# Kernel optimization log

Hardware: AMD Instinct MI355X
Metric: run time of the kernel (lower is better)

Reference implementation:

```python
import jax, jax.numpy as jnp
import numpy as np

FP8_MAX = 448.0
FP8_HI_PREC_MAX = 224.0
UNC_THRESH = 0.1
EPS = 1e-08


def setup_inputs() -> dict:
    key = jax.random.key(0)
    k1, k2, k3 = jax.random.split(key, 3)
    B, S, H, D, M = 1, 4096, 32, 128, 4096
    return {
        "k": jax.random.normal(k1, (B, S, H, D), dtype=jnp.float32),
        "v": jax.random.normal(k2, (B, S, H, D), dtype=jnp.float32),
        "uncertainty": jax.random.uniform(k3, (B, S), dtype=jnp.float32),
        "k_cache": jnp.zeros((H, M, D), dtype=jnp.float32),
        "v_cache": jnp.zeros((H, M, D), dtype=jnp.float32),
        "k_scales": jnp.ones((H, M), dtype=jnp.float32),
        "v_scales": jnp.ones((H, M), dtype=jnp.float32),
        "current_pos": 0,
    }


def reference(k, v, uncertainty, k_cache, v_cache, k_scales, v_scales, current_pos):
    # k, v: [1, S, H, D]; caches: [H, M, D]; scales: [H, M]
    H, M, D = k_cache.shape
    S = k.shape[1]
    pos = (current_pos + jnp.arange(S)) % M  # circular-buffer write positions

    kt = k[0]  # [S, H, D]
    vt = v[0]

    # per-token fp8 divisor: high-precision range when uncertain
    div = jnp.where(uncertainty[0] > UNC_THRESH, FP8_HI_PREC_MAX, FP8_MAX)  # [S]

    # per-token amax over all heads and dims -> scalar scale per token
    k_s = jnp.maximum(jnp.max(jnp.abs(kt), axis=(1, 2)) / div, EPS)  # [S]
    v_s = jnp.maximum(jnp.max(jnp.abs(vt), axis=(1, 2)) / div, EPS)

    kq = jnp.clip(kt / k_s[:, None, None], -FP8_MAX, FP8_MAX)  # [S, H, D]
    vq = jnp.clip(vt / v_s[:, None, None], -FP8_MAX, FP8_MAX)

    # scatter-append into circular buffer ([H, S, D] layout for cache writes)
    new_k_cache = k_cache.at[:, pos].set(jnp.swapaxes(kq, 0, 1))
    new_v_cache = v_cache.at[:, pos].set(jnp.swapaxes(vq, 0, 1))
    new_k_scales = k_scales.at[:, pos].set(jnp.broadcast_to(k_s, (H, S)))
    new_v_scales = v_scales.at[:, pos].set(jnp.broadcast_to(v_s, (H, S)))
    return (new_k_cache, new_v_cache, new_k_scales, new_v_scales)
```

## Files before the change

kernel.cpp:

```cpp
#include <hip/hip_runtime.h>

#define HH 32
#define DD 128
#define MM 4096
#define ROW_F4 1024
#define D_F4   32

typedef float v4f __attribute__((ext_vector_type(4)));

__global__ __launch_bounds__(256)
void teleport_quant_kernel(const float* __restrict__ kin,
                           const float* __restrict__ vin,
                           const float* __restrict__ unc,
                           const float* __restrict__ kc_in,
                           const float* __restrict__ vc_in,
                           const float* __restrict__ ksc_in,
                           const float* __restrict__ vsc_in,
                           const int*   __restrict__ cur_pos,
                           float* __restrict__ kc_out,
                           float* __restrict__ vc_out,
                           float* __restrict__ ksc_out,
                           float* __restrict__ vsc_out,
                           int S)
{
    const int t    = threadIdx.x;
    const int lane = t & 63;
    const int w    = (blockIdx.x << 2) + (t >> 6);
    const int m    = w >> 1;
    const int isV  = w & 1;

    int cp  = *cur_pos;
    int cpm = cp % MM; if (cpm < 0) cpm += MM;
    int s0  = m - cpm; if (s0 < 0) s0 += MM;
    const int s = (s0 < S) ? (s0 + MM * ((S - 1 - s0) / MM)) : -1;

    const v4f* cin  = reinterpret_cast<const v4f*>(isV ? vc_in : kc_in);
    v4f*       cout = reinterpret_cast<v4f*>(isV ? vc_out : kc_out);
    const float* sin_ = isV ? vsc_in  : ksc_in;
    float*       sout = isV ? vsc_out : ksc_out;

    if (s < 0) {
        #pragma unroll
        for (int c = 0; c < 16; ++c) {
            int f4 = c * 64 + lane;
            int o  = (f4 >> 5) * (MM * D_F4) + m * D_F4 + (f4 & 31);
            cout[o] = cin[o];
        }
        if (lane < HH) sout[lane * MM + m] = sin_[lane * MM + m];
        return;
    }

    const v4f* src = reinterpret_cast<const v4f*>(isV ? vin : kin)
                     + (size_t)s * ROW_F4;

    v4f a[16];
    float am = 0.0f;
    #pragma unroll
    for (int c = 0; c < 16; ++c) {
        a[c] = src[c * 64 + lane];
        am = fmaxf(am, fmaxf(fmaxf(fabsf(a[c].x), fabsf(a[c].y)),
                             fmaxf(fabsf(a[c].z), fabsf(a[c].w))));
    }

    #pragma unroll
    for (int off = 32; off > 0; off >>= 1)
        am = fmaxf(am, __shfl_xor(am, off, 64));

    const float u   = unc[s];
    const float div = (u > 0.1f) ? 224.0f : 448.0f;
    const float sc  = fmaxf(am / div, 1e-8f);
    const float r   = 1.0f / sc;

    #pragma unroll
    for (int c = 0; c < 16; ++c) {
        int f4 = c * 64 + lane;
        int o  = (f4 >> 5) * (MM * D_F4) + m * D_F4 + (f4 & 31);
        v4f q;
        q.x = fminf(fmaxf(a[c].x * r, -448.0f), 448.0f);
        q.y = fminf(fmaxf(a[c].y * r, -448.0f), 448.0f);
        q.z = fminf(fmaxf(a[c].z * r, -448.0f), 448.0f);
        q.w = fminf(fmaxf(a[c].w * r, -448.0f), 448.0f);
        cout[o] = q;
    }

    if (lane < HH) sout[lane * MM + m] = sc;
}

extern "C" void kernel_launch(void* const* d_in, const int* in_sizes, int n_in,
                              void* d_out, int out_size, void* d_ws, size_t ws_size,
                              hipStream_t stream) {
    const float* kin = (const float*)d_in[0];
    const float* vin = (const float*)d_in[1];
    const float* unc = (const float*)d_in[2];
    const float* kc  = (const float*)d_in[3];
    const float* vc  = (const float*)d_in[4];
    const float* ksc = (const float*)d_in[5];
    const float* vsc = (const float*)d_in[6];
    const int*   cp  = (const int*)d_in[7];
    const int S = in_sizes[2];

    float* out  = (float*)d_out;
    float* kco  = out;
    float* vco  = kco + (size_t)HH * MM * DD;
    float* ksco = vco + (size_t)HH * MM * DD;
    float* vsco = ksco + (size_t)HH * MM;

    teleport_quant_kernel<<<(2 * MM) / 4, 256, 0, stream>>>(
        kin, vin, unc, kc, vc, ksc, vsc, cp, kco, vco, ksco, vsco, S);
}
```

Before: 51.86 us.

## Split quantization into scale pass and head-major write pass

Splits the fused kernel into two launches. The first computes per-token scales and reciprocals into workspace; the second reads k/v again and writes the cache in contiguous head-major order. This targets the strided scatter writes of the original per-token layout, at the cost of reading inputs twice and an extra launch.

Result: slower. 69.66 us (+34.3%).

```diff
diff --git a/kernel.cpp b/kernel.cpp
--- a/kernel.cpp
+++ b/kernel.cpp
@@ -9,19 +9,13 @@
 typedef float v4f __attribute__((ext_vector_type(4)));
 
 __global__ __launch_bounds__(256)
-void teleport_quant_kernel(const float* __restrict__ kin,
-                           const float* __restrict__ vin,
-                           const float* __restrict__ unc,
-                           const float* __restrict__ kc_in,
-                           const float* __restrict__ vc_in,
-                           const float* __restrict__ ksc_in,
-                           const float* __restrict__ vsc_in,
-                           const int*   __restrict__ cur_pos,
-                           float* __restrict__ kc_out,
-                           float* __restrict__ vc_out,
-                           float* __restrict__ ksc_out,
-                           float* __restrict__ vsc_out,
-                           int S)
+void pass_scales(const float* __restrict__ kin,
+                 const float* __restrict__ vin,
+                 const float* __restrict__ unc,
+                 const int*   __restrict__ cur_pos,
+                 float* __restrict__ ws_sc,
+                 float* __restrict__ ws_r,
+                 int S)
 {
     const int t    = threadIdx.x;
     const int lane = t & 63;
@@ -32,58 +26,92 @@
     int cp  = *cur_pos;
     int cpm = cp % MM; if (cpm < 0) cpm += MM;
     int s0  = m - cpm; if (s0 < 0) s0 += MM;
-    const int s = (s0 < S) ? (s0 + MM * ((S - 1 - s0) / MM)) : -1;
-
-    const v4f* cin  = reinterpret_cast<const v4f*>(isV ? vc_in : kc_in);
-    v4f*       cout = reinterpret_cast<v4f*>(isV ? vc_out : kc_out);
-    const float* sin_ = isV ? vsc_in  : ksc_in;
-    float*       sout = isV ? vsc_out : ksc_out;
-
-    if (s < 0) {
-        #pragma unroll
-        for (int c = 0; c < 16; ++c) {
-            int f4 = c * 64 + lane;
-            int o  = (f4 >> 5) * (MM * D_F4) + m * D_F4 + (f4 & 31);
-            cout[o] = cin[o];
-        }
-        if (lane < HH) sout[lane * MM + m] = sin_[lane * MM + m];
-        return;
-    }
+    const int s = (s0 < S) ? (s0 + MM * ((S - 1 - s0) >> 12)) : -1;
+    if (s < 0) return;
 
     const v4f* src = reinterpret_cast<const v4f*>(isV ? vin : kin)
                      + (size_t)s * ROW_F4;
-
-    v4f a[16];
     float am = 0.0f;
     #pragma unroll
     for (int c = 0; c < 16; ++c) {
-        a[c] = src[c * 64 + lane];
-        am = fmaxf(am, fmaxf(fmaxf(fabsf(a[c].x), fabsf(a[c].y)),
-                             fmaxf(fabsf(a[c].z), fabsf(a[c].w))));
+        v4f a = src[c * 64 + lane];
+        am = fmaxf(am, fmaxf(fmaxf(fabsf(a.x), fabsf(a.y)),
+                             fmaxf(fabsf(a.z), fabsf(a.w))));
     }
-
     #pragma unroll
     for (int off = 32; off > 0; off >>= 1)
         am = fmaxf(am, __shfl_xor(am, off, 64));
 
-    const float u   = unc[s];
-    const float div = (u > 0.1f) ? 224.0f : 448.0f;
-    const float sc  = fmaxf(am / div, 1e-8f);
-    const float r   = 1.0f / sc;
+    if (lane == 0) {
+        const float u   = unc[s];
+        const float div = (u > 0.1f) ? 224.0f : 448.0f;
+        const float sc  = fmaxf(am / div, 1e-8f);
+        ws_sc[isV * MM + m] = sc;
+        ws_r [isV * MM + m] = 1.0f / sc;
+    }
+}
+
+__global__ __launch_bounds__(256)
+void pass_quant(const float* __restrict__ kin,
+                const float* __restrict__ vin,
+                const float* __restrict__ kc_in,
+                const float* __restrict__ vc_in,
+                const float* __restrict__ ksc_in,
+                const float* __restrict__ vsc_in,
+                const int*   __restrict__ cur_pos,
+                float* __restrict__ kc_out,
+                float* __restrict__ vc_out,
+                float* __restrict__ ksc_out,
+                float* __restrict__ vsc_out,
+                const float* __restrict__ ws_sc,
+                const float* __restrict__ ws_r,
+                int S)
+{
+    const int t    = threadIdx.x;
+    const int lane = t & 63;
+    const int w    = (blockIdx.x << 2) + (t >> 6);
+    const int isV  = w >> 12;
+    const int wt   = w & 4095;
+    const int h    = wt >> 7;
+    const int mb   = (wt & 127) << 5;
+    const int d4   = lane & 31;
+    const int half = lane >> 5;
+
+    const v4f*  in_  = reinterpret_cast<const v4f*>(isV ? vin : kin);
+    const v4f*  cin  = reinterpret_cast<const v4f*>(isV ? vc_in : kc_in);
+    v4f*        cout = reinterpret_cast<v4f*>(isV ? vc_out : kc_out);
+    const float* sin_ = isV ? vsc_in  : ksc_in;
+    float*       sout = isV ? vsc_out : ksc_out;
+    const float* wsc  = ws_sc + isV * MM;
+    const float* wr   = ws_r  + isV * MM;
+
+    int cp  = *cur_pos;
+    int cpm = cp % MM; if (cpm < 0) cpm += MM;
+
+    v4f* outbase = cout + (size_t)h * (MM * D_F4) + (size_t)mb * D_F4;
 
     #pragma unroll
-    for (int c = 0; c < 16; ++c) {
-        int f4 = c * 64 + lane;
-        int o  = (f4 >> 5) * (MM * D_F4) + m * D_F4 + (f4 & 31);
+    for (int i = 0; i < 16; ++i) {
+        const int m  = mb + 2 * i + half;
+        int s0 = m - cpm; if (s0 < 0) s0 += MM;
+        const int s = (s0 < S) ? (s0 + MM * ((S - 1 - s0) >> 12)) : -1;
+
+        const int rel = (2 * i + half) * D_F4 + d4;
         v4f q;
-        q.x = fminf(fmaxf(a[c].x * r, -448.0f), 448.0f);
-        q.y = fminf(fmaxf(a[c].y * r, -448.0f), 448.0f);
-        q.z = fminf(fmaxf(a[c].z * r, -448.0f), 448.0f);
-        q.w = fminf(fmaxf(a[c].w * r, -448.0f), 448.0f);
-        cout[o] = q;
+        if (s >= 0) {
+            v4f val = in_[(size_t)s * ROW_F4 + h * D_F4 + d4];
+            const float r = wr[m];
+            q.x = fminf(fmaxf(val.x * r, -448.0f), 448.0f);
+            q.y = fminf(fmaxf(val.y * r, -448.0f), 448.0f);
+            q.z = fminf(fmaxf(val.z * r, -448.0f), 448.0f);
+            q.w = fminf(fmaxf(val.w * r, -448.0f), 448.0f);
+            if (d4 == 0) sout[h * MM + m] = wsc[m];
+        } else {
+            q = cin[(size_t)h * (MM * D_F4) + (size_t)m * D_F4 + d4];
+            if (d4 == 0) sout[h * MM + m] = sin_[h * MM + m];
+        }
+        outbase[rel] = q;
     }
-
-    if (lane < HH) sout[lane * MM + m] = sc;
 }
 
 extern "C" void kernel_launch(void* const* d_in, const int* in_sizes, int n_in,
@@ -105,6 +133,12 @@
     float* ksco = vco + (size_t)HH * MM * DD;
     float* vsco = ksco + (size_t)HH * MM;
 
-    teleport_quant_kernel<<<(2 * MM) / 4, 256, 0, stream>>>(
-        kin, vin, unc, kc, vc, ksc, vsc, cp, kco, vco, ksco, vsco, S);
+    float* ws_sc = (float*)d_ws;
+    float* ws_r  = ws_sc + 2 * MM;
+
+    pass_scales<<<(2 * MM) / 4, 256, 0, stream>>>(
+        kin, vin, unc, cp, ws_sc, ws_r, S);
+
+    pass_quant<<<(2 * MM * 2) / 4 / 2 * 2 / 2, 256, 0, stream>>>(
+        kin, vin, kc, vc, ksc, vsc, cp, kco, vco, ksco, vsco, ws_sc, ws_r, S);
 }
```

## Stage token rows in LDS via direct global-to-LDS loads and rewrite stores

Applied to the files above, without the earlier changes.

Each block now handles four consecutive cache slots for either K or V. Rows are staged into shared memory with global_load_lds, bypassing registers. After a per-wave amax reduction, the block writes out with threads remapped so that four adjacent slots form contiguous 2KB chunks per head, instead of 512B chunks per wave. This aims to improve store coalescing and cut register pressure, at the cost of 64KB LDS per block, which limits occupancy, plus a block-wide barrier.

After: 49.67 us. -4.2%, faster.

```diff
diff --git a/kernel.cpp b/kernel.cpp
--- a/kernel.cpp
+++ b/kernel.cpp
@@ -5,85 +5,124 @@
 #define MM 4096
 #define ROW_F4 1024
 #define D_F4   32
+#define TPB    4
 
 typedef float v4f __attribute__((ext_vector_type(4)));
 
+__device__ __forceinline__ void gl_lds16(const v4f* g, v4f* l) {
+    __builtin_amdgcn_global_load_lds(
+        (const __attribute__((address_space(1))) unsigned int*)g,
+        (__attribute__((address_space(3))) unsigned int*)l,
+        16, 0, 0);
+}
+
+__device__ __forceinline__ int src_token(int m, int cpm, int S) {
+    int s0 = m - cpm; if (s0 < 0) s0 += MM;
+    return (s0 < S) ? (s0 + MM * ((S - 1 - s0) / MM)) : -1;
+}
+
 __global__ __launch_bounds__(256)
-void teleport_quant_kernel(const float* __restrict__ kin,
-                           const float* __restrict__ vin,
-                           const float* __restrict__ unc,
-                           const float* __restrict__ kc_in,
-                           const float* __restrict__ vc_in,
-                           const float* __restrict__ ksc_in,
-                           const float* __restrict__ vsc_in,
-                           const int*   __restrict__ cur_pos,
-                           float* __restrict__ kc_out,
-                           float* __restrict__ vc_out,
-                           float* __restrict__ ksc_out,
-                           float* __restrict__ vsc_out,
-                           int S)
+void teleport_fused(const float* __restrict__ kin,
+                    const float* __restrict__ vin,
+                    const float* __restrict__ unc,
+                    const float* __restrict__ kc_in,
+                    const float* __restrict__ vc_in,
+                    const float* __restrict__ ksc_in,
+                    const float* __restrict__ vsc_in,
+                    const int*   __restrict__ cur_pos,
+                    float* __restrict__ kc_out,
+                    float* __restrict__ vc_out,
+                    float* __restrict__ ksc_out,
+                    float* __restrict__ vsc_out,
+                    int S)
 {
+    __shared__ v4f   sh[TPB * ROW_F4];
+    __shared__ float sc_l[TPB];
+
     const int t    = threadIdx.x;
     const int lane = t & 63;
-    const int w    = (blockIdx.x << 2) + (t >> 6);
-    const int m    = w >> 1;
-    const int isV  = w & 1;
+    const int wv   = t >> 6;
+    const int b    = blockIdx.x;
+    const int isV  = b >> 10;
+    const int mb   = (b & 1023) * TPB;
+
+    const float* in_  = isV ? vin : kin;
+    const float* cin  = isV ? vc_in : kc_in;
+    float*       cout = isV ? vc_out : kc_out;
+    const float* sin_ = isV ? vsc_in  : ksc_in;
+    float*       sout = isV ? vsc_out : ksc_out;
 
     int cp  = *cur_pos;
     int cpm = cp % MM; if (cpm < 0) cpm += MM;
-    int s0  = m - cpm; if (s0 < 0) s0 += MM;
-    const int s = (s0 < S) ? (s0 + MM * ((S - 1 - s0) / MM)) : -1;
 
-    const v4f* cin  = reinterpret_cast<const v4f*>(isV ? vc_in : kc_in);
-    v4f*       cout = reinterpret_cast<v4f*>(isV ? vc_out : kc_out);
-    const float* sin_ = isV ? vsc_in  : ksc_in;
-    float*       sout = isV ? vsc_out : ksc_out;
-
-    if (s < 0) {
+    const int m = mb + wv;
+    const int s = src_token(m, cpm, S);
+    if (s >= 0) {
+        const v4f* src = reinterpret_cast<const v4f*>(in_) + (size_t)s * ROW_F4;
+        #pragma unroll
+        for (int c = 0; c < 16; ++c)
+            gl_lds16(src + c * 64 + lane, sh + wv * ROW_F4 + c * 64);
+    } else {
+        const v4f* cb = reinterpret_cast<const v4f*>(cin);
         #pragma unroll
         for (int c = 0; c < 16; ++c) {
             int f4 = c * 64 + lane;
-            int o  = (f4 >> 5) * (MM * D_F4) + m * D_F4 + (f4 & 31);
-            cout[o] = cin[o];
+            gl_lds16(cb + (size_t)(f4 >> 5) * (MM * D_F4) + (size_t)m * D_F4 + (f4 & 31),
+                     sh + wv * ROW_F4 + c * 64);
         }
-        if (lane < HH) sout[lane * MM + m] = sin_[lane * MM + m];
-        return;
+    }
+    asm volatile("s_waitcnt vmcnt(0)" ::: "memory");
+
+    if (s >= 0) {
+        float am = 0.0f;
+        #pragma unroll
+        for (int c = 0; c < 16; ++c) {
+            v4f a = sh[wv * ROW_F4 + c * 64 + lane];
+            am = fmaxf(am, fmaxf(fmaxf(fabsf(a.x), fabsf(a.y)),
+                                 fmaxf(fabsf(a.z), fabsf(a.w))));
+        }
+        #pragma unroll
+        for (int off = 32; off > 0; off >>= 1)
+            am = fmaxf(am, __shfl_xor(am, off, 64));
+        if (lane == 0) {
+            const float u   = unc[s];
+            const float div = (u > 0.1f) ? 224.0f : 448.0f;
+            sc_l[wv] = fmaxf(am / div, 1e-8f);
+        }
+    }
+    __syncthreads();
+
+    const int ml   = (t >> 5) & (TPB - 1);
+    const int d4   = t & 31;
+    const int hoff = t >> 7;
+    const int mq   = mb + ml;
+    const int sq   = src_token(mq, cpm, S);
+    const float r  = (sq >= 0) ? (1.0f / sc_l[ml]) : 1.0f;
+
+    v4f* coutv = reinterpret_cast<v4f*>(cout);
+    #pragma unroll
+    for (int i = 0; i < 16; ++i) {
+        const int h = 2 * i + hoff;
+        v4f a = sh[ml * ROW_F4 + h * D_F4 + d4];
+        v4f q;
+        if (sq >= 0) {
+            q.x = fminf(fmaxf(a.x * r, -448.0f), 448.0f);
+            q.y = fminf(fmaxf(a.y * r, -448.0f), 448.0f);
+            q.z = fminf(fmaxf(a.z * r, -448.0f), 448.0f);
+            q.w = fminf(fmaxf(a.w * r, -448.0f), 448.0f);
+        } else {
+            q = a;
+        }
+        coutv[(size_t)h * (MM * D_F4) + (size_t)mq * D_F4 + d4] = q;
     }
 
-    const v4f* src = reinterpret_cast<const v4f*>(isV ? vin : kin)
-                     + (size_t)s * ROW_F4;
-
-    v4f a[16];
-    float am = 0.0f;
-    #pragma unroll
-    for (int c = 0; c < 16; ++c) {
-        a[c] = src[c * 64 + lane];
-        am = fmaxf(am, fmaxf(fmaxf(fabsf(a[c].x), fabsf(a[c].y)),
-                             fmaxf(fabsf(a[c].z), fabsf(a[c].w))));
+    if (t < 128) {
+        const int h   = t >> 2;
+        const int mll = t & 3;
+        const int msc = mb + mll;
+        const int ss  = src_token(msc, cpm, S);
+        sout[h * MM + msc] = (ss >= 0) ? sc_l[mll] : sin_[h * MM + msc];
     }
-
-    #pragma unroll
-    for (int off = 32; off > 0; off >>= 1)
-        am = fmaxf(am, __shfl_xor(am, off, 64));
-
-    const float u   = unc[s];
-    const float div = (u > 0.1f) ? 224.0f : 448.0f;
-    const float sc  = fmaxf(am / div, 1e-8f);
-    const float r   = 1.0f / sc;
-
-    #pragma unroll
-    for (int c = 0; c < 16; ++c) {
-        int f4 = c * 64 + lane;
-        int o  = (f4 >> 5) * (MM * D_F4) + m * D_F4 + (f4 & 31);
-        v4f q;
-        q.x = fminf(fmaxf(a[c].x * r, -448.0f), 448.0f);
-        q.y = fminf(fmaxf(a[c].y * r, -448.0f), 448.0f);
-        q.z = fminf(fmaxf(a[c].z * r, -448.0f), 448.0f);
-        q.w = fminf(fmaxf(a[c].w * r, -448.0f), 448.0f);
-        cout[o] = q;
-    }
-
-    if (lane < HH) sout[lane * MM + m] = sc;
 }
 
 extern "C" void kernel_launch(void* const* d_in, const int* in_sizes, int n_in,
@@ -105,6 +144,6 @@
     float* ksco = vco + (size_t)HH * MM * DD;
     float* vsco = ksco + (size_t)HH * MM;
 
-    teleport_quant_kernel<<<(2 * MM) / 4, 256, 0, stream>>>(
+    teleport_fused<<<2 * (MM / TPB), 256, 0, stream>>>(
         kin, vin, unc, kc, vc, ksc, vsc, cp, kco, vco, ksco, vsco, S);
 }
```
